# Kernel optimization log

Measured on AMD Instinct MI355X. Metric: run time of the kernel, lower is better.

Reference implementation:

```python
import jax, jax.numpy as jnp
import numpy as np

N, K, E = 50000, 8, 800000
HID, OUT, DIM_PE, DIM_IN, DIM_EMB = 64, 16, 16, 64, 128

def setup_inputs() -> dict:
    key = jax.random.key(0)
    ks = jax.random.split(key, 16)
    s = 0.05
    inp = {
        "eigvecs": jax.random.normal(ks[0], (N, K), jnp.float32),
        "x": jax.random.normal(ks[1], (N, DIM_IN), jnp.float32),
        "edge_index": jax.random.randint(ks[2], (2, E), 0, N, jnp.int32),
        "batch_index": jnp.sort(jax.random.randint(ks[3], (N,), 0, 8, jnp.int32)),
        # GIN layer 0: MLP(1 -> HID, 1 layer) == single Linear
        "W0": jax.random.normal(ks[4], (1, HID), jnp.float32) * s,
        "b0": jnp.zeros((HID,), jnp.float32),
        # GIN layer 1: MLP(HID -> HID, 1 layer)
        "W1": jax.random.normal(ks[5], (HID, HID), jnp.float32) * s,
        "b1": jnp.zeros((HID,), jnp.float32),
        # GIN layer 2: MLP(HID -> HID -> OUT, 2 layers, relu between)
        "W2a": jax.random.normal(ks[6], (HID, HID), jnp.float32) * s,
        "b2a": jnp.zeros((HID,), jnp.float32),
        "W2b": jax.random.normal(ks[7], (HID, OUT), jnp.float32) * s,
        "b2b": jnp.zeros((OUT,), jnp.float32),
        # rho: MLP(OUT*K -> HID -> DIM_PE, 2 layers)
        "Wr1": jax.random.normal(ks[8], (OUT * K, HID), jnp.float32) * s,
        "br1": jnp.zeros((HID,), jnp.float32),
        "Wr2": jax.random.normal(ks[9], (HID, DIM_PE), jnp.float32) * s,
        "br2": jnp.zeros((DIM_PE,), jnp.float32),
        # linear_x: dim_in -> dim_emb - dim_pe
        "Wx": jax.random.normal(ks[10], (DIM_IN, DIM_EMB - DIM_PE), jnp.float32) * s,
        "bx": jnp.zeros((DIM_EMB - DIM_PE,), jnp.float32),
    }
    return inp

def reference(eigvecs, x, edge_index, batch_index,
              W0, b0, W1, b1, W2a, b2a, W2b, b2b,
              Wr1, br1, Wr2, br2, Wx, bx):
    src, dst = edge_index[0], edge_index[1]

    def agg(h):
        # GINConv sum aggregation: out[i] = h[i] + sum_{(j->i) in E} h[j]  (eps=0)
        return h + jax.ops.segment_sum(h[src], dst, num_segments=N)

    def enc(p):
        # p: [N, K, C]; Linear acts on last dim, message passing on node dim 0
        h = agg(p) @ W0 + b0                       # GINConv(MLP 1-layer): [N,K,HID]
        h = agg(h) @ W1 + b1                       # GINConv(MLP 1-layer)
        m = agg(h)
        return jax.nn.relu(m @ W2a + b2a) @ W2b + b2b  # GINConv(MLP 2-layer): [N,K,OUT]

    # pos_enc = eigvecs.unsqueeze(-1), NaN -> 0
    pos = jnp.nan_to_num(eigvecs)[:, :, None]      # [N,K,1]
    pe = enc(pos) + enc(-pos)                      # sign-invariant sum: [N,K,OUT]
    pe = pe.reshape(N, K * OUT)                    # [N, K*OUT]
    pe = jax.nn.relu(pe @ Wr1 + br1) @ Wr2 + br2   # rho MLP: [N, DIM_PE]

    h = x.astype(jnp.float32) @ Wx + bx            # expand_x linear: [N, DIM_EMB-DIM_PE]
    return jnp.concatenate([h, pe], axis=1)        # [N, DIM_EMB]
```

## Files before the change

kernel.cpp:

```cpp
#include <hip/hip_runtime.h>

#define NCH 9

__global__ void smallvec_k(const float* __restrict__ W0, const float* __restrict__ b0,
                           const float* __restrict__ W1, const float* __restrict__ b1,
                           const float* __restrict__ W2a, float* __restrict__ SV) {
  __shared__ float w01[64], g[64];
  int j = threadIdx.x;
  float a = 0.f, bg = 0.f;
  for (int i = 0; i < 64; ++i) { float w = W1[i*64 + j]; a += W0[i]*w; bg += b0[i]*w; }
  w01[j] = a; g[j] = bg;
  __syncthreads();
  float w012 = 0.f, P = 0.f, Q = 0.f;
  for (int i = 0; i < 64; ++i) { float w = W2a[i*64 + j]; w012 += w01[i]*w; P += g[i]*w; Q += b1[i]*w; }
  SV[j] = w012; SV[64 + j] = P; SV[128 + j] = Q;
}

__global__ void zero_k(int* __restrict__ p, int n) {
  int i = blockIdx.x * blockDim.x + threadIdx.x;
  if (i < n) p[i] = 0;
}

__global__ void hist_k(const int* __restrict__ ei, int* __restrict__ cnt, int E) {
  int e = blockIdx.x * blockDim.x + threadIdx.x;
  if (e < E) atomicAdd(&cnt[ei[E + e]], 1);
}

__global__ void scan_k(int* __restrict__ ptr, int* __restrict__ cur, int N) {
  __shared__ int sums[256];
  int t = threadIdx.x;
  int chunk = (N + 255) / 256;
  int lo = t * chunk, hi = lo + chunk; if (hi > N) hi = N; if (lo > N) lo = N;
  int s = 0;
  for (int i = lo; i < hi; ++i) s += ptr[i];
  sums[t] = s;
  __syncthreads();
  for (int off = 1; off < 256; off <<= 1) {
    int v = (t >= off) ? sums[t - off] : 0;
    __syncthreads();
    sums[t] += v;
    __syncthreads();
  }
  int run = sums[t] - s;
  for (int i = lo; i < hi; ++i) {
    int c = ptr[i];
    ptr[i] = run; cur[i] = run;
    run += c;
  }
  if (t == 255) ptr[N] = run;
}

__global__ void fill_k(const int* __restrict__ ei, int* __restrict__ cur,
                       int* __restrict__ csr, int E) {
  int e = blockIdx.x * blockDim.x + threadIdx.x;
  if (e >= E) return;
  int s = ei[e], d = ei[E + e];
  int pos = atomicAdd(&cur[d], 1);
  csr[pos] = s;
}

__global__ void agg1_k(const int* __restrict__ ptr, const int* __restrict__ csr,
                       const float* __restrict__ eig, float* __restrict__ B1, int N) {
  int idx = blockIdx.x * blockDim.x + threadIdx.x;
  if (idx >= N * NCH) return;
  int n = idx / NCH, ch = idx % NCH;
  int lo = ptr[n], hi = ptr[n + 1];
  if (ch == 8) { B1[idx] = 1.f + (float)(hi - lo); return; }
  float v = eig[(size_t)n * 8 + ch]; v = (v != v) ? 0.f : v;
  float acc = v;
  int j = lo;
  for (; j + 4 <= hi; j += 4) {
    int s0 = csr[j], s1 = csr[j+1], s2 = csr[j+2], s3 = csr[j+3];
    float u0 = eig[(size_t)s0*8 + ch], u1 = eig[(size_t)s1*8 + ch];
    float u2 = eig[(size_t)s2*8 + ch], u3 = eig[(size_t)s3*8 + ch];
    u0 = (u0!=u0)?0.f:u0; u1 = (u1!=u1)?0.f:u1; u2 = (u2!=u2)?0.f:u2; u3 = (u3!=u3)?0.f:u3;
    acc += u0 + u1 + u2 + u3;
  }
  for (; j < hi; ++j) {
    int s = csr[j];
    float u = eig[(size_t)s*8 + ch]; u = (u!=u)?0.f:u;
    acc += u;
  }
  B1[idx] = acc;
}

template<int CHO>
__global__ void agg_k(const int* __restrict__ ptr, const int* __restrict__ csr,
                      const float* __restrict__ Bin, float* __restrict__ Bout, int N) {
  int idx = blockIdx.x * blockDim.x + threadIdx.x;
  if (idx >= N * CHO) return;
  int n = idx / CHO, ch = idx % CHO;
  int lo = ptr[n], hi = ptr[n + 1];
  float acc = Bin[(size_t)n * NCH + ch];
  int j = lo;
  for (; j + 4 <= hi; j += 4) {
    int s0 = csr[j], s1 = csr[j+1], s2 = csr[j+2], s3 = csr[j+3];
    acc += Bin[(size_t)s0*NCH + ch] + Bin[(size_t)s1*NCH + ch]
         + Bin[(size_t)s2*NCH + ch] + Bin[(size_t)s3*NCH + ch];
  }
  for (; j < hi; ++j) acc += Bin[(size_t)csr[j]*NCH + ch];
  Bout[idx] = acc;
}

__global__ __launch_bounds__(256) void pe_k(
    const float* __restrict__ B1, const float* __restrict__ B2, const float* __restrict__ B3,
    const float* __restrict__ SV, const float* __restrict__ b2a,
    const float* __restrict__ W2b, const float* __restrict__ b2b,
    const float* __restrict__ Wr1, const float* __restrict__ br1,
    const float* __restrict__ Wr2, const float* __restrict__ br2,
    float* __restrict__ out, int N) {
  __shared__ float vbuf[4][8][64];
  __shared__ float pebuf[4][128];
  __shared__ float zbuf[4][64];
  int wid  = threadIdx.x >> 6;
  int lane = threadIdx.x & 63;
  int n = blockIdx.x * 4 + wid;
  bool active = (n < N);
  float d1 = 0.f, d2 = 0.f;
  if (active) { d1 = B1[(size_t)n*NCH + 8]; d2 = B2[(size_t)n*NCH + 8]; }
  float w012 = SV[lane], P = SV[64 + lane], Q = SV[128 + lane];
  float Ej = d2 * P + d1 * Q + b2a[lane];
  if (active) {
    #pragma unroll
    for (int k = 0; k < 8; ++k) {
      float s = B3[(size_t)n*8 + k];
      float t = s * w012;
      vbuf[wid][k][lane] = fmaxf(t + Ej, 0.f) + fmaxf(Ej - t, 0.f);
    }
  }
  __syncthreads();
  if (active) {
    #pragma unroll
    for (int cc = 0; cc < 2; ++cc) {
      int c = lane + cc * 64;
      int k = c >> 4, o = c & 15;
      float acc = 2.f * b2b[o];
      #pragma unroll 8
      for (int j = 0; j < 64; ++j) acc += vbuf[wid][k][j] * W2b[j*16 + o];
      pebuf[wid][c] = acc;
    }
  }
  __syncthreads();
  float acc = br1[lane];
  if (active) {
    #pragma unroll 8
    for (int c = 0; c < 128; ++c) acc += pebuf[wid][c] * Wr1[c*64 + lane];
    zbuf[wid][lane] = fmaxf(acc, 0.f);
  }
  __syncthreads();
  if (active && lane < 16) {
    float acc2 = br2[lane];
    #pragma unroll 8
    for (int h = 0; h < 64; ++h) acc2 += zbuf[wid][h] * Wr2[h*16 + lane];
    out[(size_t)n*128 + 112 + lane] = acc2;
  }
}

__global__ void x_k(const float* __restrict__ x, const float* __restrict__ Wx,
                    const float* __restrict__ bx, float* __restrict__ out, int total) {
  int idx = blockIdx.x * blockDim.x + threadIdx.x;
  if (idx >= total) return;
  int n = idx / 112, o = idx % 112;
  const float* xr = x + (size_t)n * 64;
  float acc = bx[o];
  #pragma unroll 8
  for (int i = 0; i < 64; ++i) acc += xr[i] * Wx[i*112 + o];
  out[(size_t)n*128 + o] = acc;
}

extern "C" void kernel_launch(void* const* d_in, const int* in_sizes, int n_in,
                              void* d_out, int out_size, void* d_ws, size_t ws_size,
                              hipStream_t stream) {
  const float* eig = (const float*)d_in[0];
  const float* x   = (const float*)d_in[1];
  const int*   ei  = (const int*)d_in[2];
  const float* W0  = (const float*)d_in[4];
  const float* b0  = (const float*)d_in[5];
  const float* W1  = (const float*)d_in[6];
  const float* b1  = (const float*)d_in[7];
  const float* W2a = (const float*)d_in[8];
  const float* b2a = (const float*)d_in[9];
  const float* W2b = (const float*)d_in[10];
  const float* b2b = (const float*)d_in[11];
  const float* Wr1 = (const float*)d_in[12];
  const float* br1 = (const float*)d_in[13];
  const float* Wr2 = (const float*)d_in[14];
  const float* br2 = (const float*)d_in[15];
  const float* Wx  = (const float*)d_in[16];
  const float* bx  = (const float*)d_in[17];
  float* out = (float*)d_out;

  int N = in_sizes[0] / 8;
  int E = in_sizes[2] / 2;

  int*   ptr = (int*)d_ws;
  int*   cur = ptr + (N + 1);
  int*   csr = cur + N;
  float* B1  = (float*)(csr + E);
  float* B2  = B1 + (size_t)N * NCH;
  float* B3  = B2 + (size_t)N * NCH;
  float* SV  = B3 + (size_t)N * 8;

  int eblocks = (E + 255) / 256;

  zero_k<<<(N + 256) / 256, 256, 0, stream>>>(ptr, N + 1);
  hist_k<<<eblocks, 256, 0, stream>>>(ei, ptr, E);
  scan_k<<<1, 256, 0, stream>>>(ptr, cur, N);
  fill_k<<<eblocks, 256, 0, stream>>>(ei, cur, csr, E);

  smallvec_k<<<1, 64, 0, stream>>>(W0, b0, W1, b1, W2a, SV);

  agg1_k<<<(N * NCH + 255) / 256, 256, 0, stream>>>(ptr, csr, eig, B1, N);
  agg_k<NCH><<<(N * NCH + 255) / 256, 256, 0, stream>>>(ptr, csr, B1, B2, N);
  agg_k<8><<<(N * 8 + 255) / 256, 256, 0, stream>>>(ptr, csr, B2, B3, N);

  pe_k<<<(N + 3) / 4, 256, 0, stream>>>(B1, B2, B3, SV, b2a, W2b, b2b,
                                        Wr1, br1, Wr2, br2, out, N);
  x_k<<<(N * 112 + 255) / 256, 256, 0, stream>>>(x, Wx, bx, out, N * 112);
}
```

Before: 538.8 us.

## Vectorize CSR aggregation with 16-lane node groups and split degree arrays

Replaces the per-(node, channel) scalar gather kernels with one templated kernel that gives each node a group of 16 lanes. Each lane strides over the neighbor list and loads a whole 8-float row as two float4, and the group combines its partial sums with shuffles. The degree channel moves out of the 9-wide rows into separate D1/D2 arrays so feature rows become 32-byte aligned. The aim is fewer redundant csr/ptr reads and better coalesced, vectorized gathers, at the cost of shuffle reductions and idle lanes on low-degree nodes. It also pads the pe_k shared buffer.

Result: no change. 544.2 us (+1.0%).

```diff
diff --git a/kernel.cpp b/kernel.cpp
--- a/kernel.cpp
+++ b/kernel.cpp
@@ -1,6 +1,4 @@
 #include <hip/hip_runtime.h>
-
-#define NCH 9
 
 __global__ void smallvec_k(const float* __restrict__ W0, const float* __restrict__ b0,
                            const float* __restrict__ W1, const float* __restrict__ b1,
@@ -59,57 +57,56 @@
   csr[pos] = s;
 }
 
-__global__ void agg1_k(const int* __restrict__ ptr, const int* __restrict__ csr,
-                       const float* __restrict__ eig, float* __restrict__ B1, int N) {
-  int idx = blockIdx.x * blockDim.x + threadIdx.x;
-  if (idx >= N * NCH) return;
-  int n = idx / NCH, ch = idx % NCH;
-  int lo = ptr[n], hi = ptr[n + 1];
-  if (ch == 8) { B1[idx] = 1.f + (float)(hi - lo); return; }
-  float v = eig[(size_t)n * 8 + ch]; v = (v != v) ? 0.f : v;
-  float acc = v;
-  int j = lo;
-  for (; j + 4 <= hi; j += 4) {
-    int s0 = csr[j], s1 = csr[j+1], s2 = csr[j+2], s3 = csr[j+3];
-    float u0 = eig[(size_t)s0*8 + ch], u1 = eig[(size_t)s1*8 + ch];
-    float u2 = eig[(size_t)s2*8 + ch], u3 = eig[(size_t)s3*8 + ch];
-    u0 = (u0!=u0)?0.f:u0; u1 = (u1!=u1)?0.f:u1; u2 = (u2!=u2)?0.f:u2; u3 = (u3!=u3)?0.f:u3;
-    acc += u0 + u1 + u2 + u3;
-  }
-  for (; j < hi; ++j) {
+#define RED16(v) { v += __shfl_down(v, 8, 16); v += __shfl_down(v, 4, 16); \
+                   v += __shfl_down(v, 2, 16); v += __shfl_down(v, 1, 16); }
+#define NANFIX4(u) { u.x = (u.x!=u.x)?0.f:u.x; u.y = (u.y!=u.y)?0.f:u.y; \
+                     u.z = (u.z!=u.z)?0.f:u.z; u.w = (u.w!=u.w)?0.f:u.w; }
+
+template<int MODE>
+__global__ __launch_bounds__(256) void aggv_k(
+    const int* __restrict__ ptr, const int* __restrict__ csr,
+    const float* __restrict__ Fin, const float* __restrict__ Din,
+    float* __restrict__ Fout, float* __restrict__ Dout, int N) {
+  int g = blockIdx.x * 16 + (threadIdx.x >> 4);
+  int t = threadIdx.x & 15;
+  if (g >= N) return;
+  int lo = ptr[g], hi = ptr[g + 1];
+  float a0=0.f,a1=0.f,a2=0.f,a3=0.f,a4=0.f,a5=0.f,a6=0.f,a7=0.f,dd=0.f;
+  for (int j = lo + t; j < hi; j += 16) {
     int s = csr[j];
-    float u = eig[(size_t)s*8 + ch]; u = (u!=u)?0.f:u;
-    acc += u;
-  }
-  B1[idx] = acc;
-}
-
-template<int CHO>
-__global__ void agg_k(const int* __restrict__ ptr, const int* __restrict__ csr,
-                      const float* __restrict__ Bin, float* __restrict__ Bout, int N) {
-  int idx = blockIdx.x * blockDim.x + threadIdx.x;
-  if (idx >= N * CHO) return;
-  int n = idx / CHO, ch = idx % CHO;
-  int lo = ptr[n], hi = ptr[n + 1];
-  float acc = Bin[(size_t)n * NCH + ch];
-  int j = lo;
-  for (; j + 4 <= hi; j += 4) {
-    int s0 = csr[j], s1 = csr[j+1], s2 = csr[j+2], s3 = csr[j+3];
-    acc += Bin[(size_t)s0*NCH + ch] + Bin[(size_t)s1*NCH + ch]
-         + Bin[(size_t)s2*NCH + ch] + Bin[(size_t)s3*NCH + ch];
-  }
-  for (; j < hi; ++j) acc += Bin[(size_t)csr[j]*NCH + ch];
-  Bout[idx] = acc;
+    const float* r = Fin + (size_t)s * 8;
+    float4 u0 = *(const float4*)r;
+    float4 u1 = *(const float4*)(r + 4);
+    if (MODE == 0) { NANFIX4(u0); NANFIX4(u1); }
+    a0 += u0.x; a1 += u0.y; a2 += u0.z; a3 += u0.w;
+    a4 += u1.x; a5 += u1.y; a6 += u1.z; a7 += u1.w;
+    if (MODE == 1) dd += Din[s];
+  }
+  RED16(a0); RED16(a1); RED16(a2); RED16(a3);
+  RED16(a4); RED16(a5); RED16(a6); RED16(a7);
+  if (MODE == 1) RED16(dd);
+  if (t == 0) {
+    const float* r = Fin + (size_t)g * 8;
+    float4 s0 = *(const float4*)r;
+    float4 s1 = *(const float4*)(r + 4);
+    if (MODE == 0) { NANFIX4(s0); NANFIX4(s1); }
+    float4 o0 = { a0 + s0.x, a1 + s0.y, a2 + s0.z, a3 + s0.w };
+    float4 o1 = { a4 + s1.x, a5 + s1.y, a6 + s1.z, a7 + s1.w };
+    *(float4*)(Fout + (size_t)g * 8)     = o0;
+    *(float4*)(Fout + (size_t)g * 8 + 4) = o1;
+    if (MODE == 0) Dout[g] = 1.f + (float)(hi - lo);
+    if (MODE == 1) Dout[g] = Din[g] + dd;
+  }
 }
 
 __global__ __launch_bounds__(256) void pe_k(
-    const float* __restrict__ B1, const float* __restrict__ B2, const float* __restrict__ B3,
+    const float* __restrict__ B3, const float* __restrict__ D1, const float* __restrict__ D2,
     const float* __restrict__ SV, const float* __restrict__ b2a,
     const float* __restrict__ W2b, const float* __restrict__ b2b,
     const float* __restrict__ Wr1, const float* __restrict__ br1,
     const float* __restrict__ Wr2, const float* __restrict__ br2,
     float* __restrict__ out, int N) {
-  __shared__ float vbuf[4][8][64];
+  __shared__ float vbuf[4][8][68];
   __shared__ float pebuf[4][128];
   __shared__ float zbuf[4][64];
   int wid  = threadIdx.x >> 6;
@@ -117,7 +114,7 @@
   int n = blockIdx.x * 4 + wid;
   bool active = (n < N);
   float d1 = 0.f, d2 = 0.f;
-  if (active) { d1 = B1[(size_t)n*NCH + 8]; d2 = B2[(size_t)n*NCH + 8]; }
+  if (active) { d1 = D1[n]; d2 = D2[n]; }
   float w012 = SV[lane], P = SV[64 + lane], Q = SV[128 + lane];
   float Ej = d2 * P + d1 * Q + b2a[lane];
   if (active) {
@@ -193,15 +190,20 @@
   int N = in_sizes[0] / 8;
   int E = in_sizes[2] / 2;
 
-  int*   ptr = (int*)d_ws;
-  int*   cur = ptr + (N + 1);
-  int*   csr = cur + N;
-  float* B1  = (float*)(csr + E);
-  float* B2  = B1 + (size_t)N * NCH;
-  float* B3  = B2 + (size_t)N * NCH;
-  float* SV  = B3 + (size_t)N * 8;
+  int* ptr = (int*)d_ws;
+  int* cur = ptr + (N + 1);
+  int* csr = cur + N;
+  uintptr_t p = (uintptr_t)(csr + E);
+  p = (p + 255) & ~(uintptr_t)255;
+  float* B1 = (float*)p;
+  float* B2 = B1 + (size_t)N * 8;
+  float* B3 = B2 + (size_t)N * 8;
+  float* D1 = B3 + (size_t)N * 8;
+  float* D2 = D1 + N;
+  float* SV = D2 + N;
 
   int eblocks = (E + 255) / 256;
+  int nblocks16 = (N + 15) / 16;
 
   zero_k<<<(N + 256) / 256, 256, 0, stream>>>(ptr, N + 1);
   hist_k<<<eblocks, 256, 0, stream>>>(ei, ptr, E);
@@ -210,11 +212,11 @@
 
   smallvec_k<<<1, 64, 0, stream>>>(W0, b0, W1, b1, W2a, SV);
 
-  agg1_k<<<(N * NCH + 255) / 256, 256, 0, stream>>>(ptr, csr, eig, B1, N);
-  agg_k<NCH><<<(N * NCH + 255) / 256, 256, 0, stream>>>(ptr, csr, B1, B2, N);
-  agg_k<8><<<(N * 8 + 255) / 256, 256, 0, stream>>>(ptr, csr, B2, B3, N);
-
-  pe_k<<<(N + 3) / 4, 256, 0, stream>>>(B1, B2, B3, SV, b2a, W2b, b2b,
+  aggv_k<0><<<nblocks16, 256, 0, stream>>>(ptr, csr, eig, nullptr, B1, D1, N);
+  aggv_k<1><<<nblocks16, 256, 0, stream>>>(ptr, csr, B1, D1, B2, D2, N);
+  aggv_k<2><<<nblocks16, 256, 0, stream>>>(ptr, csr, B2, nullptr, B3, nullptr, N);
+
+  pe_k<<<(N + 3) / 4, 256, 0, stream>>>(B3, D1, D2, SV, b2a, W2b, b2b,
                                         Wr1, br1, Wr2, br2, out, N);
   x_k<<<(N * 112 + 255) / 256, 256, 0, stream>>>(x, Wx, bx, out, N * 112);
 }
```
